# Kernel optimization log

Measured on AMD Instinct MI355X. Metric: run time of the kernel, lower is better.

Reference implementation:

```python
import jax, jax.numpy as jnp
import numpy as np

SIGMA = 1e-4
GAMMA = 1e-4
ZNEAR = 1.0
ZFAR = 100.0
EPS = 1e-10

N, H, W, K = 4, 256, 256, 8
V, F, D = 6890, 13776, 16


def setup_inputs() -> dict:
    key = jax.random.key(0)
    k1, k2, k3, k4, k5, k6 = jax.random.split(key, 6)
    vert_features = jax.random.normal(k1, (V, D), dtype=jnp.float32)
    # barycentric coords: positive, sum to 1 over last axis
    b = jax.random.uniform(k2, (N, H, W, K, 3), dtype=jnp.float32, minval=1e-3, maxval=1.0)
    bary_coords = b / jnp.sum(b, axis=-1, keepdims=True)
    # 2D pixel-to-face distances, on the scale of sigma
    dists = jax.random.normal(k3, (N, H, W, K), dtype=jnp.float32) * 1e-4
    # depths within [znear, zfar]
    zbuf = jax.random.uniform(k4, (N, H, W, K), dtype=jnp.float32, minval=ZNEAR, maxval=ZFAR)
    faces = jax.random.randint(k5, (F, 3), 0, V, dtype=jnp.int64)
    # -1 marks pixels not covered by a face (background)
    pix_to_face = jax.random.randint(k6, (N, H, W, K), -1, F, dtype=jnp.int64)
    return {
        "vert_features": vert_features,
        "bary_coords": bary_coords,
        "dists": dists,
        "zbuf": zbuf,
        "faces": faces,
        "pix_to_face": pix_to_face,
    }


def _interpolate_face_attributes(pix_to_face, bary_coords, face_attrs):
    # face_attrs: (F, 3, D); pix_to_face: (N,H,W,K); bary: (N,H,W,K,3)
    idx = jnp.clip(pix_to_face, 0, face_attrs.shape[0] - 1)
    gathered = face_attrs[idx]  # (N,H,W,K,3,D)
    pix = jnp.einsum("nhwkv,nhwkvd->nhwkd", bary_coords, gathered)
    valid = (pix_to_face >= 0).astype(pix.dtype)[..., None]
    return pix * valid  # (N,H,W,K,D)


def _softmax_feature_blend(features, pix_to_face, dists, zbuf, background):
    # features: (N,H,W,K,D)
    dt = features.dtype
    mask = (pix_to_face >= 0).astype(dt)  # (N,H,W,K)
    prob_map = jax.nn.sigmoid(-dists / (SIGMA + 1e-8)) * mask
    alpha = 1.0 - jnp.prod(1.0 - prob_map, axis=-1)  # (N,H,W)
    z_inv = (ZFAR - zbuf) / (ZFAR - ZNEAR) * mask
    z_inv_max = jnp.clip(jnp.max(z_inv, axis=-1, keepdims=True), EPS, None)
    weights_num = prob_map * jnp.exp((z_inv - z_inv_max) / GAMMA)
    delta = jnp.clip(jnp.exp((EPS - z_inv_max) / GAMMA), EPS, None)  # (N,H,W,1)
    denom = jnp.sum(weights_num, axis=-1, keepdims=True) + delta
    weighted = jnp.einsum("nhwk,nhwkd->nhwd", weights_num, features)
    pix = (weighted + delta * background) / denom
    return jnp.concatenate([pix, alpha[..., None]], axis=-1)  # (N,H,W,D+1)


def reference(vert_features, bary_coords, dists, zbuf, faces, pix_to_face):
    face_attrs = vert_features[faces]  # (F,3,D) gather via packed faces
    pix_feats = _interpolate_face_attributes(pix_to_face, bary_coords, face_attrs)
    background = jnp.zeros((vert_features.shape[-1],), dtype=vert_features.dtype)
    out = _softmax_feature_blend(pix_feats, pix_to_face, dists, zbuf, background)
    # (N, D+1, H, W) to mirror the permute((0,3,1,2)) in forward_interpolate
    return jnp.transpose(out, (0, 3, 1, 2))
```

## Files before the change

kernel.cpp:

```cpp
#include <hip/hip_runtime.h>
#include <math.h>

namespace {
constexpr int Nn = 4, Hh = 256, Ww = 256;
constexpr int HW = Hh * Ww;
constexpr int P  = Nn * HW;
constexpr float ZFAR  = 100.0f;
constexpr float ZNEAR = 1.0f;
constexpr float INV_SIG = 1.0f / (1e-4f + 1e-8f);
constexpr float INV_GAM = 1.0f / 1e-4f;
constexpr float EPSF    = 1e-10f;
constexpr float INV_ZR  = 1.0f / (ZFAR - ZNEAR);
}

#define FMA4(A, C, Rp, i)                                   \
    {                                                       \
        float4 _t = (Rp)[i];                                \
        A.x = fmaf((C), _t.x, A.x);                         \
        A.y = fmaf((C), _t.y, A.y);                         \
        A.z = fmaf((C), _t.z, A.z);                         \
        A.w = fmaf((C), _t.w, A.w);                         \
    }

__global__ __launch_bounds__(256) void render_kernel(
    const float* __restrict__ vf,
    const float* __restrict__ bary,
    const float* __restrict__ dists,
    const float* __restrict__ zbuf,
    const int*  __restrict__ faces,
    const int*  __restrict__ p2f,
    float* __restrict__ out)
{
    const int p = blockIdx.x * blockDim.x + threadIdx.x;
    if (p >= P) return;

    const int4*   fp = reinterpret_cast<const int4*>(p2f + (size_t)p * 8);
    const float4* zp = reinterpret_cast<const float4*>(zbuf + (size_t)p * 8);
    const float4* dp = reinterpret_cast<const float4*>(dists + (size_t)p * 8);
    const float4* bp = reinterpret_cast<const float4*>(bary + (size_t)p * 24);
    int4   fA = fp[0], fB = fp[1];
    float4 zA = zp[0], zB = zp[1];
    float4 dA = dp[0], dB = dp[1];
    float4 b0 = bp[0], b1 = bp[1], b2 = bp[2], b3 = bp[3], b4 = bp[4], b5 = bp[5];

    int fk[8] = {fA.x, fA.y, fA.z, fA.w, fB.x, fB.y, fB.z, fB.w};
    float zraw[8] = {zA.x, zA.y, zA.z, zA.w, zB.x, zB.y, zB.z, zB.w};
    float dk[8] = {dA.x, dA.y, dA.z, dA.w, dB.x, dB.y, dB.z, dB.w};
    float bc[24] = {b0.x, b0.y, b0.z, b0.w,
                    b1.x, b1.y, b1.z, b1.w,
                    b2.x, b2.y, b2.z, b2.w,
                    b3.x, b3.y, b3.z, b3.w,
                    b4.x, b4.y, b4.z, b4.w,
                    b5.x, b5.y, b5.z, b5.w};

    float zi[8];
    float zmax = EPSF;
#pragma unroll
    for (int k = 0; k < 8; ++k) {
        const bool valid = fk[k] >= 0;
        float zv = valid ? (ZFAR - zraw[k]) * INV_ZR : 0.0f;
        zi[k] = zv;
        zmax = fmaxf(zmax, zv);
    }

    const float delta = fmaxf(__expf((EPSF - zmax) * INV_GAM), EPSF);
    float denom = delta;
    float keep  = 1.0f;
    float wv[8];
#pragma unroll
    for (int k = 0; k < 8; ++k) {
        const bool valid = fk[k] >= 0;
        float pr = valid ? 1.0f / (1.0f + __expf(dk[k] * INV_SIG)) : 0.0f;
        keep *= (1.0f - pr);
        float w = pr * __expf((zi[k] - zmax) * INV_GAM);
        wv[k] = w;
        denom += w;
    }

    float4 acc0 = make_float4(0.f, 0.f, 0.f, 0.f);
    float4 acc1 = make_float4(0.f, 0.f, 0.f, 0.f);
    float4 acc2 = make_float4(0.f, 0.f, 0.f, 0.f);
    float4 acc3 = make_float4(0.f, 0.f, 0.f, 0.f);

    while (true) {
        float wb = 0.0f, s0 = 0.0f, s1 = 0.0f, s2 = 0.0f;
        int fsel = 0, ksel = -1;
#pragma unroll
        for (int k = 0; k < 8; ++k) {
            const bool better = wv[k] > wb;
            wb   = better ? wv[k] : wb;
            fsel = better ? fk[k] : fsel;
            ksel = better ? k : ksel;
            s0   = better ? bc[k * 3 + 0] : s0;
            s1   = better ? bc[k * 3 + 1] : s1;
            s2   = better ? bc[k * 3 + 2] : s2;
        }
        if (!__any(wb > 0.0f)) break;

        if (wb > 0.0f) {
            const int4 vidx = *reinterpret_cast<const int4*>(faces + (size_t)fsel * 3);
            const float c0 = wb * s0;
            const float c1 = wb * s1;
            const float c2 = wb * s2;
            const float4* r0 = reinterpret_cast<const float4*>(vf + (size_t)vidx.x * 16);
            const float4* r1 = reinterpret_cast<const float4*>(vf + (size_t)vidx.y * 16);
            const float4* r2 = reinterpret_cast<const float4*>(vf + (size_t)vidx.z * 16);
            FMA4(acc0, c0, r0, 0); FMA4(acc1, c0, r0, 1);
            FMA4(acc2, c0, r0, 2); FMA4(acc3, c0, r0, 3);
            FMA4(acc0, c1, r1, 0); FMA4(acc1, c1, r1, 1);
            FMA4(acc2, c1, r1, 2); FMA4(acc3, c1, r1, 3);
            FMA4(acc0, c2, r2, 0); FMA4(acc1, c2, r2, 1);
            FMA4(acc2, c2, r2, 2); FMA4(acc3, c2, r2, 3);
        }

#pragma unroll
        for (int k = 0; k < 8; ++k)
            wv[k] = (ksel == k) ? 0.0f : wv[k];
    }

    const float invden = 1.0f / denom;
    const int n  = p >> 16;
    const int hw = p & (HW - 1);
    float* o = out + (size_t)n * 17 * HW + hw;
    o[(size_t)0  * HW] = acc0.x * invden;
    o[(size_t)1  * HW] = acc0.y * invden;
    o[(size_t)2  * HW] = acc0.z * invden;
    o[(size_t)3  * HW] = acc0.w * invden;
    o[(size_t)4  * HW] = acc1.x * invden;
    o[(size_t)5  * HW] = acc1.y * invden;
    o[(size_t)6  * HW] = acc1.z * invden;
    o[(size_t)7  * HW] = acc1.w * invden;
    o[(size_t)8  * HW] = acc2.x * invden;
    o[(size_t)9  * HW] = acc2.y * invden;
    o[(size_t)10 * HW] = acc2.z * invden;
    o[(size_t)11 * HW] = acc2.w * invden;
    o[(size_t)12 * HW] = acc3.x * invden;
    o[(size_t)13 * HW] = acc3.y * invden;
    o[(size_t)14 * HW] = acc3.z * invden;
    o[(size_t)15 * HW] = acc3.w * invden;
    o[(size_t)16 * HW] = 1.0f - keep;
}

extern "C" void kernel_launch(void* const* d_in, const int* in_sizes, int n_in,
                              void* d_out, int out_size, void* d_ws, size_t ws_size,
                              hipStream_t stream) {
    const float* vf    = (const float*)d_in[0];
    const float* bary  = (const float*)d_in[1];
    const float* dists = (const float*)d_in[2];
    const float* zbuf  = (const float*)d_in[3];
    const int*   faces = (const int*)d_in[4];
    const int*   p2f   = (const int*)d_in[5];
    float* out = (float*)d_out;

    render_kernel<<<dim3(P / 256), dim3(256), 0, stream>>>(
        vf, bary, dists, zbuf, faces, p2f, out);
}
```

Baseline: 23.68 us.

## Share vertex-feature gathers across quads via DPP and transpose through LDS

Within each group of four lanes, each lane broadcasts its selected face's vertex indices and weights to the other lanes with DPP quad permutes. Each lane then loads only one float4 quarter of each vertex row for all four pixels, so a quad makes coalesced 64-byte row reads instead of scattered per-pixel 64-byte reads. The partial sums are transposed back through shared memory with a block barrier. Barycentric coordinates are now loaded on demand per selected slot rather than all up front. This adds four serialized DPP slot passes per iteration, extra LDS traffic, and a __syncthreads.

```diff
diff --git a/kernel.cpp b/kernel.cpp
--- a/kernel.cpp
+++ b/kernel.cpp
@@ -8,18 +8,32 @@
 constexpr float ZFAR  = 100.0f;
 constexpr float ZNEAR = 1.0f;
 constexpr float INV_SIG = 1.0f / (1e-4f + 1e-8f);
-constexpr float INV_GAM = 1.0f / 1e-4f;
+constexpr float INV_GAM = 1e4f;
 constexpr float EPSF    = 1e-10f;
 constexpr float INV_ZR  = 1.0f / (ZFAR - ZNEAR);
 }
 
-#define FMA4(A, C, Rp, i)                                   \
-    {                                                       \
-        float4 _t = (Rp)[i];                                \
-        A.x = fmaf((C), _t.x, A.x);                         \
-        A.y = fmaf((C), _t.y, A.y);                         \
-        A.z = fmaf((C), _t.z, A.z);                         \
-        A.w = fmaf((C), _t.w, A.w);                         \
+#define QB_I(v, S) __builtin_amdgcn_mov_dpp((v), ((S) * 0x55), 0xf, 0xf, true)
+#define QB_F(v, S) __int_as_float(QB_I(__float_as_int(v), S))
+
+#define DO_SLOT(S, PS)                                                         \
+    {                                                                          \
+        const float ws = QB_F(wb, S);                                          \
+        if (ws > 0.0f) {                                                       \
+            const int   g0 = QB_I(vx, S);                                      \
+            const int   g1 = QB_I(vy, S);                                      \
+            const int   g2 = QB_I(vz, S);                                      \
+            const float w0 = QB_F(c0, S);                                      \
+            const float w1 = QB_F(c1, S);                                      \
+            const float w2 = QB_F(c2, S);                                      \
+            const float4 r0 = *(reinterpret_cast<const float4*>(vf + (size_t)g0 * 16) + cq); \
+            const float4 r1 = *(reinterpret_cast<const float4*>(vf + (size_t)g1 * 16) + cq); \
+            const float4 r2 = *(reinterpret_cast<const float4*>(vf + (size_t)g2 * 16) + cq); \
+            PS.x = fmaf(w0, r0.x, fmaf(w1, r1.x, fmaf(w2, r2.x, PS.x)));       \
+            PS.y = fmaf(w0, r0.y, fmaf(w1, r1.y, fmaf(w2, r2.y, PS.y)));       \
+            PS.z = fmaf(w0, r0.z, fmaf(w1, r1.z, fmaf(w2, r2.z, PS.z)));       \
+            PS.w = fmaf(w0, r0.w, fmaf(w1, r1.w, fmaf(w2, r2.w, PS.w)));       \
+        }                                                                      \
     }
 
 __global__ __launch_bounds__(256) void render_kernel(
@@ -31,27 +45,22 @@
     const int*  __restrict__ p2f,
     float* __restrict__ out)
 {
-    const int p = blockIdx.x * blockDim.x + threadIdx.x;
-    if (p >= P) return;
+    __shared__ float xp[256 * 20];
+    const int pp = threadIdx.x;
+    const int p  = blockIdx.x * 256 + pp;
+    const int cq = pp & 3;
+    const int qb = pp & ~3;
 
     const int4*   fp = reinterpret_cast<const int4*>(p2f + (size_t)p * 8);
     const float4* zp = reinterpret_cast<const float4*>(zbuf + (size_t)p * 8);
     const float4* dp = reinterpret_cast<const float4*>(dists + (size_t)p * 8);
-    const float4* bp = reinterpret_cast<const float4*>(bary + (size_t)p * 24);
     int4   fA = fp[0], fB = fp[1];
     float4 zA = zp[0], zB = zp[1];
     float4 dA = dp[0], dB = dp[1];
-    float4 b0 = bp[0], b1 = bp[1], b2 = bp[2], b3 = bp[3], b4 = bp[4], b5 = bp[5];
 
     int fk[8] = {fA.x, fA.y, fA.z, fA.w, fB.x, fB.y, fB.z, fB.w};
     float zraw[8] = {zA.x, zA.y, zA.z, zA.w, zB.x, zB.y, zB.z, zB.w};
     float dk[8] = {dA.x, dA.y, dA.z, dA.w, dB.x, dB.y, dB.z, dB.w};
-    float bc[24] = {b0.x, b0.y, b0.z, b0.w,
-                    b1.x, b1.y, b1.z, b1.w,
-                    b2.x, b2.y, b2.z, b2.w,
-                    b3.x, b3.y, b3.z, b3.w,
-                    b4.x, b4.y, b4.z, b4.w,
-                    b5.x, b5.y, b5.z, b5.w};
 
     float zi[8];
     float zmax = EPSF;
@@ -77,13 +86,13 @@
         denom += w;
     }
 
-    float4 acc0 = make_float4(0.f, 0.f, 0.f, 0.f);
-    float4 acc1 = make_float4(0.f, 0.f, 0.f, 0.f);
-    float4 acc2 = make_float4(0.f, 0.f, 0.f, 0.f);
-    float4 acc3 = make_float4(0.f, 0.f, 0.f, 0.f);
+    float4 ps0 = make_float4(0.f, 0.f, 0.f, 0.f);
+    float4 ps1 = make_float4(0.f, 0.f, 0.f, 0.f);
+    float4 ps2 = make_float4(0.f, 0.f, 0.f, 0.f);
+    float4 ps3 = make_float4(0.f, 0.f, 0.f, 0.f);
 
     while (true) {
-        float wb = 0.0f, s0 = 0.0f, s1 = 0.0f, s2 = 0.0f;
+        float wb = 0.0f;
         int fsel = 0, ksel = -1;
 #pragma unroll
         for (int k = 0; k < 8; ++k) {
@@ -91,53 +100,58 @@
             wb   = better ? wv[k] : wb;
             fsel = better ? fk[k] : fsel;
             ksel = better ? k : ksel;
-            s0   = better ? bc[k * 3 + 0] : s0;
-            s1   = better ? bc[k * 3 + 1] : s1;
-            s2   = better ? bc[k * 3 + 2] : s2;
         }
         if (!__any(wb > 0.0f)) break;
 
+        int vx = 0, vy = 0, vz = 0;
+        float c0 = 0.0f, c1 = 0.0f, c2 = 0.0f;
         if (wb > 0.0f) {
             const int4 vidx = *reinterpret_cast<const int4*>(faces + (size_t)fsel * 3);
-            const float c0 = wb * s0;
-            const float c1 = wb * s1;
-            const float c2 = wb * s2;
-            const float4* r0 = reinterpret_cast<const float4*>(vf + (size_t)vidx.x * 16);
-            const float4* r1 = reinterpret_cast<const float4*>(vf + (size_t)vidx.y * 16);
-            const float4* r2 = reinterpret_cast<const float4*>(vf + (size_t)vidx.z * 16);
-            FMA4(acc0, c0, r0, 0); FMA4(acc1, c0, r0, 1);
-            FMA4(acc2, c0, r0, 2); FMA4(acc3, c0, r0, 3);
-            FMA4(acc0, c1, r1, 0); FMA4(acc1, c1, r1, 1);
-            FMA4(acc2, c1, r1, 2); FMA4(acc3, c1, r1, 3);
-            FMA4(acc0, c2, r2, 0); FMA4(acc1, c2, r2, 1);
-            FMA4(acc2, c2, r2, 2); FMA4(acc3, c2, r2, 3);
+            const float4 bq = *reinterpret_cast<const float4*>(bary + (size_t)p * 24 + ksel * 3);
+            vx = vidx.x; vy = vidx.y; vz = vidx.z;
+            c0 = wb * bq.x; c1 = wb * bq.y; c2 = wb * bq.z;
         }
+
+        DO_SLOT(0, ps0)
+        DO_SLOT(1, ps1)
+        DO_SLOT(2, ps2)
+        DO_SLOT(3, ps3)
 
 #pragma unroll
         for (int k = 0; k < 8; ++k)
-            wv[k] = (ksel == k) ? 0.0f : wv[k];
+            wv[k] = (k == ksel) ? 0.0f : wv[k];
     }
+
+    *reinterpret_cast<float4*>(&xp[(qb + 0) * 20 + cq * 4]) = ps0;
+    *reinterpret_cast<float4*>(&xp[(qb + 1) * 20 + cq * 4]) = ps1;
+    *reinterpret_cast<float4*>(&xp[(qb + 2) * 20 + cq * 4]) = ps2;
+    *reinterpret_cast<float4*>(&xp[(qb + 3) * 20 + cq * 4]) = ps3;
+    __syncthreads();
+    const float4 a0 = *reinterpret_cast<const float4*>(&xp[pp * 20 + 0]);
+    const float4 a1 = *reinterpret_cast<const float4*>(&xp[pp * 20 + 4]);
+    const float4 a2 = *reinterpret_cast<const float4*>(&xp[pp * 20 + 8]);
+    const float4 a3 = *reinterpret_cast<const float4*>(&xp[pp * 20 + 12]);
 
     const float invden = 1.0f / denom;
     const int n  = p >> 16;
     const int hw = p & (HW - 1);
     float* o = out + (size_t)n * 17 * HW + hw;
-    o[(size_t)0  * HW] = acc0.x * invden;
-    o[(size_t)1  * HW] = acc0.y * invden;
-    o[(size_t)2  * HW] = acc0.z * invden;
-    o[(size_t)3  * HW] = acc0.w * invden;
-    o[(size_t)4  * HW] = acc1.x * invden;
-    o[(size_t)5  * HW] = acc1.y * invden;
-    o[(size_t)6  * HW] = acc1.z * invden;
-    o[(size_t)7  * HW] = acc1.w * invden;
-    o[(size_t)8  * HW] = acc2.x * invden;
-    o[(size_t)9  * HW] = acc2.y * invden;
-    o[(size_t)10 * HW] = acc2.z * invden;
-    o[(size_t)11 * HW] = acc2.w * invden;
-    o[(size_t)12 * HW] = acc3.x * invden;
-    o[(size_t)13 * HW] = acc3.y * invden;
-    o[(size_t)14 * HW] = acc3.z * invden;
-    o[(size_t)15 * HW] = acc3.w * invden;
+    o[(size_t)0  * HW] = a0.x * invden;
+    o[(size_t)1  * HW] = a0.y * invden;
+    o[(size_t)2  * HW] = a0.z * invden;
+    o[(size_t)3  * HW] = a0.w * invden;
+    o[(size_t)4  * HW] = a1.x * invden;
+    o[(size_t)5  * HW] = a1.y * invden;
+    o[(size_t)6  * HW] = a1.z * invden;
+    o[(size_t)7  * HW] = a1.w * invden;
+    o[(size_t)8  * HW] = a2.x * invden;
+    o[(size_t)9  * HW] = a2.y * invden;
+    o[(size_t)10 * HW] = a2.z * invden;
+    o[(size_t)11 * HW] = a2.w * invden;
+    o[(size_t)12 * HW] = a3.x * invden;
+    o[(size_t)13 * HW] = a3.y * invden;
+    o[(size_t)14 * HW] = a3.z * invden;
+    o[(size_t)15 * HW] = a3.w * invden;
     o[(size_t)16 * HW] = 1.0f - keep;
 }
 
```

After: 21.17 us. 10.6% less time.
